# Performance work log

Hardware: AMD Instinct MI355X
Metric: run time of the kernel (lower is better)

The kernel has to match this reference:

```python
import jax, jax.numpy as jnp
import numpy as np

B, T, F, U = 64, 512, 32, 64
EPS = 1e-3  # keras LayerNormalization default epsilon


def _ln(x, g, b):
    m = jnp.mean(x, axis=-1, keepdims=True)
    v = jnp.var(x, axis=-1, keepdims=True)
    return (x - m) / jnp.sqrt(v + EPS) * g + b


def setup_inputs() -> dict:
    key = jax.random.key(0)
    ks = jax.random.split(key, 24)
    s = 0.05
    inp = {
        "x": jax.random.normal(ks[0], (B, T, F), dtype=jnp.float32),
        # per-feature GRNs, stacked over F (each sub-net has independent params)
        "W1": jax.random.normal(ks[1], (F, U), jnp.float32) * s,   # dense_1 (1->U)
        "b1": jnp.zeros((F, U), jnp.float32),
        "W2": jax.random.normal(ks[2], (F, U, U), jnp.float32) * s,  # dense_2 (U->U)
        "b2": jnp.zeros((F, U), jnp.float32),
        "Wg1": jax.random.normal(ks[3], (F, U, U), jnp.float32) * s,  # GLU linear
        "bg1": jnp.zeros((F, U), jnp.float32),
        "Wg2": jax.random.normal(ks[4], (F, U, U), jnp.float32) * s,  # GLU gate
        "bg2": jnp.zeros((F, U), jnp.float32),
        "Wp": jax.random.normal(ks[5], (F, U), jnp.float32) * s,   # project (1->U)
        "bp": jnp.zeros((F, U), jnp.float32),
        "gamma": jnp.ones((F, U), jnp.float32),
        "beta": jnp.zeros((F, U), jnp.float32),
        # weights GRN (F -> F, no projection since in_dim == units == F)
        "w1w": jax.random.normal(ks[6], (F, F), jnp.float32) * s,
        "b1w": jnp.zeros((F,), jnp.float32),
        "w2w": jax.random.normal(ks[7], (F, F), jnp.float32) * s,
        "b2w": jnp.zeros((F,), jnp.float32),
        "wg1w": jax.random.normal(ks[8], (F, F), jnp.float32) * s,
        "bg1w": jnp.zeros((F,), jnp.float32),
        "wg2w": jax.random.normal(ks[9], (F, F), jnp.float32) * s,
        "bg2w": jnp.zeros((F,), jnp.float32),
        "gammaw": jnp.ones((F,), jnp.float32),
        "betaw": jnp.zeros((F,), jnp.float32),
    }
    return inp


def reference(x, W1, b1, W2, b2, Wg1, bg1, Wg2, bg2, Wp, bp, gamma, beta,
              w1w, b1w, w2w, b2w, wg1w, bg1w, wg2w, bg2w, gammaw, betaw):
    # ---- variable weights GRN on flattened features (input dim F == units F, no projection) ----
    h = jax.nn.elu(jnp.einsum('btf,fg->btg', x, w1w) + b1w)
    h = jnp.einsum('btf,fg->btg', h, w2w) + b2w
    g = (jnp.einsum('btf,fg->btg', h, wg1w) + bg1w) * jax.nn.sigmoid(
        jnp.einsum('btf,fg->btg', h, wg2w) + bg2w)
    w = _ln(g + x, gammaw, betaw)
    w = jax.nn.softmax(w, axis=-1)  # [B,T,F]

    # ---- per-feature GRNs, batched over F (scalar input per feature) ----
    xe = x[..., None]                                   # [B,T,F,1]
    res = xe * Wp + bp                                  # project residual [B,T,F,U]
    h = jax.nn.elu(xe * W1 + b1)                        # dense_1 [B,T,F,U]
    h = jnp.einsum('btfu,fuv->btfv', h, W2) + b2        # dense_2
    g = (jnp.einsum('btfu,fuv->btfv', h, Wg1) + bg1) * jax.nn.sigmoid(
        jnp.einsum('btfu,fuv->btfv', h, Wg2) + bg2)     # GLU
    y = _ln(g + res, gamma, beta)                       # [B,T,F,U]

    out = jnp.einsum('btfu,btf->btu', y, w)             # softmax-weighted sum over features
    return out, w
```

## Files before the change

kernel.cpp:

```cpp
#include <hip/hip_runtime.h>
#include <hip/hip_bf16.h>


typedef float f4      __attribute__((ext_vector_type(4)));
typedef float f2      __attribute__((ext_vector_type(2)));
typedef float f32x4   __attribute__((ext_vector_type(4)));
typedef short bf16x8  __attribute__((ext_vector_type(8)));
typedef unsigned short u16x4 __attribute__((ext_vector_type(4)));
typedef unsigned short u16x8 __attribute__((ext_vector_type(8)));

#define N_ROWS 32768
#define F_DIM  32
#define U_DIM  64
#define RPB    16
#define NTHR   256
#define NBLK   (N_ROWS / RPB)

#define PHA_FRAG 49152
#define VECT_BYTE_OFF 794624

#define X_OFF   0
#define WT_OFF  2304
#define VA_OFF  3584
#define SMEM_BYTES 16384

__device__ __forceinline__ unsigned short bfu(float x) {
  union { __hip_bfloat16 h; unsigned short u; } c;
  c.h = __float2bfloat16(x);
  return c.u;
}
__device__ __forceinline__ float bf2f(unsigned short u) {
  union { float f; unsigned v; } c; c.v = ((unsigned)u) << 16; return c.f;
}

__global__ __launch_bounds__(256) void vsn_prep(
    const float* __restrict__ W2,  const float* __restrict__ Wg1, const float* __restrict__ Wg2,
    const float* __restrict__ W1,  const float* __restrict__ b1,  const float* __restrict__ b2,
    const float* __restrict__ bg1, const float* __restrict__ bg2,
    const float* __restrict__ Wp,  const float* __restrict__ bp,
    const float* __restrict__ gamma_, const float* __restrict__ beta_,
    const float* __restrict__ w1w, const float* __restrict__ w2w,
    const float* __restrict__ wg1w, const float* __restrict__ wg2w,
    unsigned short* __restrict__ wtg, float* __restrict__ vect)
{
  const int t = threadIdx.x, blk = blockIdx.x;
  if (blk < 192) {
    const int m = blk >> 6;
    const int f = (blk >> 1) & 31;
    const int half = blk & 1;
    const float* src = (m == 0) ? W2 : (m == 1) ? Wg1 : Wg2;
    src += f * 4096;
    const int c  = half * 256 + t;
    const int nt = c >> 7;
    const int rr = c & 127;
    const int kt = rr >> 6;
    const int ln = rr & 63;
    const int g  = ln >> 4, lrr = ln & 15;
    const int uo = lrr + 16 * nt;
    u16x8 tmp;
    if (m == 0) {
      #pragma unroll
      for (int j = 0; j < 8; ++j)
        tmp[j] = bfu(src[(8 * g + 32 * kt + j) * 64 + uo]);
    } else {
      #pragma unroll
      for (int j = 0; j < 8; ++j)
        tmp[j] = bfu(src[(4 * g + (j & 3) + 16 * (j >> 2) + 32 * kt) * 64 + uo]);
    }
    *(u16x8*)(wtg + ((size_t)(m * 32 + f) * 512 + c) * 8) = tmp;
  } else if (blk < 194) {
    const int h = blk - 192;
    for (int i = h * 1024 + t; i < (h + 1) * 1024; i += 256) {
      const int f = i >> 6, u = i & 63;
      float* vf = vect + f * 576;
      vf[u]              = W1[i];
      vf[64 + u]         = b1[i];
      vf[128 + u]        = b2[i];
      vf[192 + u * 4 + 0] = bg1[i];
      vf[192 + u * 4 + 1] = bg2[i];
      vf[192 + u * 4 + 2] = Wp[i];
      vf[192 + u * 4 + 3] = bp[i];
      vf[448 + u * 2 + 0] = gamma_[i];
      vf[448 + u * 2 + 1] = beta_[i];
    }
  } else {
    #pragma unroll
    for (int cc = 0; cc < 2; ++cc) {
      const int q = t + cc * 256;
      const int mat = q >> 7;
      const int nt  = (q >> 6) & 1;
      const int ln  = q & 63;
      const int lr  = ln & 15, lg = ln >> 4;
      const float* src = (mat == 0) ? w1w : (mat == 1) ? w2w : (mat == 2) ? wg1w : wg2w;
      u16x8 tmp;
      if (mat == 0) {
        #pragma unroll
        for (int j = 0; j < 8; ++j)
          tmp[j] = bfu(src[(8 * lg + j) * 32 + lr + 16 * nt]);
      } else {
        #pragma unroll
        for (int j = 0; j < 8; ++j)
          tmp[j] = bfu(src[(4 * lg + (j & 3) + 16 * (j >> 2)) * 32 + lr + 16 * nt]);
      }
      *(u16x8*)(wtg + ((size_t)PHA_FRAG + q) * 8) = tmp;
    }
  }
}

__global__ __launch_bounds__(NTHR, 4) void vsn_main(
    const float* __restrict__ x,
    const unsigned short* __restrict__ wtg,
    const float* __restrict__ vect,
    const float* __restrict__ b1w, const float* __restrict__ b2w,
    const float* __restrict__ bg1w, const float* __restrict__ bg2w,
    const float* __restrict__ gammaw, const float* __restrict__ betaw,
    float* __restrict__ out, float* __restrict__ wout)
{
  __shared__ __align__(16) char smem[SMEM_BYTES];
  const int t  = threadIdx.x;
  const int r0 = blockIdx.x * RPB;

  float* xt  = (float*)(smem + X_OFF);
  unsigned short* wtlb = (unsigned short*)(smem + WT_OFF);
  float* vAl = (float*)(smem + VA_OFF);

  const int wid  = t >> 6;
  const int lane = t & 63;
  const int lr   = lane & 15;
  const int lg   = lane >> 4;
  const int fbase = wid * 8;

  if (t < 128) {
    f4 v = ((const f4*)(x + (size_t)r0 * F_DIM))[t];
    *((f4*)(xt + (t >> 3) * 36 + ((t & 7) << 2))) = v;
  }
  if (t < 48) {
    int m = t >> 3, off = (t & 7) << 2;
    const float* src = (m==0)?b1w:(m==1)?b2w:(m==2)?bg1w:(m==3)?bg2w:(m==4)?gammaw:betaw;
    *(f4*)(vAl + m * 32 + off) = *((const f4*)(src + off));
  }
  __syncthreads();

  {
    const bf16x8* pf = ((const bf16x8*)wtg) + PHA_FRAG;

    f4 xa0 = *(const f4*)(xt + lr * 36 + 8 * lg);
    f4 xa1 = *(const f4*)(xt + lr * 36 + 8 * lg + 4);
    bf16x8 xb;
    #pragma unroll
    for (int j = 0; j < 4; ++j) { xb[j] = (short)bfu(xa0[j]); xb[4 + j] = (short)bfu(xa1[j]); }

    f32x4 c1a[2];
    #pragma unroll
    for (int nt = 0; nt < 2; ++nt)
      c1a[nt] = __builtin_amdgcn_mfma_f32_16x16x32_bf16(
          pf[(0 * 2 + nt) * 64 + lane], xb, (f32x4){0.f,0.f,0.f,0.f}, 0, 0, 0);
    float hv[8];
    #pragma unroll
    for (int nt = 0; nt < 2; ++nt)
      #pragma unroll
      for (int rg = 0; rg < 4; ++rg) {
        const int g = 4 * lg + rg + 16 * nt;
        float h = c1a[nt][rg] + vAl[g];
        hv[nt * 4 + rg] = h > 0.f ? h : (__expf(h) - 1.f);
      }
    bf16x8 hf;
    #pragma unroll
    for (int j = 0; j < 8; ++j) hf[j] = (short)bfu(hv[j]);

    f32x4 c2a[2];
    #pragma unroll
    for (int nt = 0; nt < 2; ++nt)
      c2a[nt] = __builtin_amdgcn_mfma_f32_16x16x32_bf16(
          pf[(1 * 2 + nt) * 64 + lane], hf, (f32x4){0.f,0.f,0.f,0.f}, 0, 0, 0);
    bf16x8 h2f;
    #pragma unroll
    for (int nt = 0; nt < 2; ++nt)
      #pragma unroll
      for (int rg = 0; rg < 4; ++rg) {
        const int g = 4 * lg + rg + 16 * nt;
        h2f[nt * 4 + rg] = (short)bfu(c2a[nt][rg] + vAl[32 + g]);
      }

    f32x4 cga[2], cgb[2];
    #pragma unroll
    for (int nt = 0; nt < 2; ++nt) {
      cga[nt] = __builtin_amdgcn_mfma_f32_16x16x32_bf16(
          pf[(2 * 2 + nt) * 64 + lane], h2f, (f32x4){0.f,0.f,0.f,0.f}, 0, 0, 0);
      cgb[nt] = __builtin_amdgcn_mfma_f32_16x16x32_bf16(
          pf[(3 * 2 + nt) * 64 + lane], h2f, (f32x4){0.f,0.f,0.f,0.f}, 0, 0, 0);
    }
    float zv[8];
    float s1 = 0.f, s2 = 0.f;
    #pragma unroll
    for (int nt = 0; nt < 2; ++nt)
      #pragma unroll
      for (int rg = 0; rg < 4; ++rg) {
        const int g = 4 * lg + rg + 16 * nt;
        float a = cga[nt][rg] + vAl[64 + g];
        float b = cgb[nt][rg] + vAl[96 + g];
        float sg = __builtin_amdgcn_rcpf(1.f + __expf(-b));
        float z = a * sg + xt[lr * 36 + g];
        zv[nt * 4 + rg] = z;
        s1 += z; s2 += z * z;
      }
    s1 += __shfl_xor(s1, 16, 64); s1 += __shfl_xor(s1, 32, 64);
    s2 += __shfl_xor(s2, 16, 64); s2 += __shfl_xor(s2, 32, 64);
    const float mA = s1 * 0.03125f;
    const float vA = s2 * 0.03125f - mA * mA;
    const float rsA = __builtin_amdgcn_rsqf(vA + 1e-3f);
    float yv[8], mx = -1e30f;
    #pragma unroll
    for (int nt = 0; nt < 2; ++nt)
      #pragma unroll
      for (int rg = 0; rg < 4; ++rg) {
        const int g = 4 * lg + rg + 16 * nt;
        float y = (zv[nt * 4 + rg] - mA) * rsA * vAl[128 + g] + vAl[160 + g];
        yv[nt * 4 + rg] = y;
        mx = fmaxf(mx, y);
      }
    mx = fmaxf(mx, __shfl_xor(mx, 16, 64));
    mx = fmaxf(mx, __shfl_xor(mx, 32, 64));
    float ev[8], es = 0.f;
    #pragma unroll
    for (int j = 0; j < 8; ++j) { ev[j] = __expf(yv[j] - mx); es += ev[j]; }
    es += __shfl_xor(es, 16, 64); es += __shfl_xor(es, 32, 64);
    const float inv = __builtin_amdgcn_rcpf(es);
    #pragma unroll
    for (int nt = 0; nt < 2; ++nt)
      #pragma unroll
      for (int rg = 0; rg < 4; ++rg) {
        const int g = 4 * lg + rg + 16 * nt;
        wtlb[lr * 40 + g] = bfu(ev[nt * 4 + rg] * inv);
      }
    if (t < 128) {
      const int row = t >> 3, c4 = (t & 7) << 2;
      u16x4 wq = *(const u16x4*)(wtlb + row * 40 + c4);
      f4 wo = { bf2f(wq[0]), bf2f(wq[1]), bf2f(wq[2]), bf2f(wq[3]) };
      *(f4*)(wout + (size_t)(r0 + row) * 32 + c4) = wo;
    }
  }

  const bf16x8* wf = (const bf16x8*)wtg;

  f32x4 acc[4];
  #pragma unroll
  for (int nt = 0; nt < 4; ++nt) acc[nt] = (f32x4){0.f, 0.f, 0.f, 0.f};

  for (int i = 0; i < 8; ++i) {
    const int f = fbase + i;
    const float* vb = vect + f * 576;

    const int base0 = (0 * 32 + f) * 512 + lane;
    bf16x8 w2f[8];
    #pragma unroll
    for (int nt = 0; nt < 4; ++nt)
      #pragma unroll
      for (int kt = 0; kt < 2; ++kt)
        w2f[nt * 2 + kt] = wf[base0 + nt * 128 + kt * 64];

    const float s_ = xt[lr * 36 + f];
    bf16x8 afr[2];
    #pragma unroll
    for (int kt = 0; kt < 2; ++kt) {
      const int u0 = 8 * lg + 32 * kt;
      f4 wa  = *(const f4*)(vb + u0);
      f4 wb_ = *(const f4*)(vb + u0 + 4);
      f4 ba  = *(const f4*)(vb + 64 + u0);
      f4 bb_ = *(const f4*)(vb + 64 + u0 + 4);
      bf16x8 af;
      #pragma unroll
      for (int j = 0; j < 4; ++j) {
        float h = s_ * wa[j] + ba[j];
        h = h > 0.f ? h : (__expf(h) - 1.f);
        af[j] = (short)bfu(h);
      }
      #pragma unroll
      for (int j = 0; j < 4; ++j) {
        float h = s_ * wb_[j] + bb_[j];
        h = h > 0.f ? h : (__expf(h) - 1.f);
        af[4 + j] = (short)bfu(h);
      }
      afr[kt] = af;
    }

    f32x4 c1[4];
    #pragma unroll
    for (int nt = 0; nt < 4; ++nt) {
      c1[nt] = (f32x4){0.f, 0.f, 0.f, 0.f};
      #pragma unroll
      for (int kt = 0; kt < 2; ++kt)
        c1[nt] = __builtin_amdgcn_mfma_f32_16x16x32_bf16(w2f[nt * 2 + kt], afr[kt], c1[nt], 0, 0, 0);
    }

    f4 b2q[4];
    #pragma unroll
    for (int kt = 0; kt < 2; ++kt)
      #pragma unroll
      for (int n2 = 0; n2 < 2; ++n2)
        b2q[n2 + 2 * kt] = *(const f4*)(vb + 128 + 4 * lg + 16 * n2 + 32 * kt);
    bf16x8 a2[2];
    #pragma unroll
    for (int kt = 0; kt < 2; ++kt) {
      bf16x8 af;
      #pragma unroll
      for (int j = 0; j < 8; ++j) {
        const int q = (j >> 2) + 2 * kt;
        af[j] = (short)bfu(c1[q][j & 3] + b2q[q][j & 3]);
      }
      a2[kt] = af;
    }

    const int base1 = (1 * 32 + f) * 512 + lane;
    bf16x8 bfa[8];
    #pragma unroll
    for (int nt = 0; nt < 4; ++nt)
      #pragma unroll
      for (int kt = 0; kt < 2; ++kt)
        bfa[nt * 2 + kt] = wf[base1 + nt * 128 + kt * 64];
    f32x4 ca[4], cb[4];
    #pragma unroll
    for (int nt = 0; nt < 4; ++nt) {
      ca[nt] = (f32x4){0.f,0.f,0.f,0.f};
      #pragma unroll
      for (int kt = 0; kt < 2; ++kt)
        ca[nt] = __builtin_amdgcn_mfma_f32_16x16x32_bf16(a2[kt], bfa[nt * 2 + kt], ca[nt], 0, 0, 0);
    }

    const int base2 = (2 * 32 + f) * 512 + lane;
    bf16x8 bfb[8];
    #pragma unroll
    for (int nt = 0; nt < 4; ++nt)
      #pragma unroll
      for (int kt = 0; kt < 2; ++kt)
        bfb[nt * 2 + kt] = wf[base2 + nt * 128 + kt * 64];
    #pragma unroll
    for (int nt = 0; nt < 4; ++nt) {
      cb[nt] = (f32x4){0.f,0.f,0.f,0.f};
      #pragma unroll
      for (int kt = 0; kt < 2; ++kt)
        cb[nt] = __builtin_amdgcn_mfma_f32_16x16x32_bf16(a2[kt], bfb[nt * 2 + kt], cb[nt], 0, 0, 0);
    }

    float xr[4], wr[4];
    #pragma unroll
    for (int rg = 0; rg < 4; ++rg) {
      const int rl = 4 * lg + rg;
      xr[rg] = xt[rl * 36 + f];
      wr[rg] = bf2f(wtlb[rl * 40 + f]);
    }
    float zf[4][4];
    float s1[4] = {0.f,0.f,0.f,0.f}, s2[4] = {0.f,0.f,0.f,0.f};
    #pragma unroll
    for (int nt = 0; nt < 4; ++nt) {
      const int u = lr + 16 * nt;
      f4 Q = *(const f4*)(vb + 192 + u * 4);
      #pragma unroll
      for (int rg = 0; rg < 4; ++rg) {
        float a = ca[nt][rg] + Q[0];
        float b = cb[nt][rg] + Q[1];
        float sg = __builtin_amdgcn_rcpf(1.f + __expf(-b));
        float z = a * sg + (xr[rg] * Q[2] + Q[3]);
        zf[nt][rg] = z;
        s1[rg] += z;
        s2[rg] += z * z;
      }
    }
    #pragma unroll
    for (int rg = 0; rg < 4; ++rg) {
      #pragma unroll
      for (int m = 1; m < 16; m <<= 1) {
        s1[rg] += __shfl_xor(s1[rg], m, 64);
        s2[rg] += __shfl_xor(s2[rg], m, 64);
      }
    }
    float rswr[4], nc2[4];
    #pragma unroll
    for (int rg = 0; rg < 4; ++rg) {
      float mn = s1[rg] * 0.015625f;
      float var = s2[rg] * 0.015625f - mn * mn;
      float rs = __builtin_amdgcn_rsqf(var + 1e-3f);
      rswr[rg] = rs * wr[rg];
      nc2[rg]  = -mn * rswr[rg];
    }
    #pragma unroll
    for (int nt = 0; nt < 4; ++nt) {
      const int u = lr + 16 * nt;
      f2 G = *(const f2*)(vb + 448 + u * 2);
      #pragma unroll
      for (int rg = 0; rg < 4; ++rg) {
        float tm = rswr[rg] * zf[nt][rg] + nc2[rg];
        acc[nt][rg] += G.x * tm + G.y * wr[rg];
      }
    }
  }

  __syncthreads();
  float* cmb = (float*)smem;
  #pragma unroll
  for (int nt = 0; nt < 4; ++nt)
    #pragma unroll
    for (int rg = 0; rg < 4; ++rg)
      cmb[wid * 1024 + (4 * lg + rg) * 64 + lr + 16 * nt] = acc[nt][rg];
  __syncthreads();
  {
    const f4* cmb4 = (const f4*)cmb;
    f4 o = cmb4[t] + cmb4[256 + t] + cmb4[512 + t] + cmb4[768 + t];
    ((f4*)(out + (size_t)r0 * U_DIM))[t] = o;
  }
}

extern "C" void kernel_launch(void* const* d_in, const int* in_sizes, int n_in,
                              void* d_out, int out_size, void* d_ws, size_t ws_size,
                              hipStream_t stream)
{
  (void)in_sizes; (void)n_in; (void)out_size; (void)ws_size;
  const float* x    = (const float*)d_in[0];
  const float* W1   = (const float*)d_in[1];
  const float* b1   = (const float*)d_in[2];
  const float* W2   = (const float*)d_in[3];
  const float* b2   = (const float*)d_in[4];
  const float* Wg1  = (const float*)d_in[5];
  const float* bg1  = (const float*)d_in[6];
  const float* Wg2  = (const float*)d_in[7];
  const float* bg2  = (const float*)d_in[8];
  const float* Wp   = (const float*)d_in[9];
  const float* bp   = (const float*)d_in[10];
  const float* gm   = (const float*)d_in[11];
  const float* bt   = (const float*)d_in[12];
  const float* w1w  = (const float*)d_in[13];
  const float* b1w  = (const float*)d_in[14];
  const float* w2w  = (const float*)d_in[15];
  const float* b2w  = (const float*)d_in[16];
  const float* wg1w = (const float*)d_in[17];
  const float* bg1w = (const float*)d_in[18];
  const float* wg2w = (const float*)d_in[19];
  const float* bg2w = (const float*)d_in[20];
  const float* gmw  = (const float*)d_in[21];
  const float* btw  = (const float*)d_in[22];

  unsigned short* wtg = (unsigned short*)d_ws;
  float* vect = (float*)((char*)d_ws + VECT_BYTE_OFF);

  float* out  = (float*)d_out;
  float* wout = out + (size_t)N_ROWS * U_DIM;

  vsn_prep<<<195, 256, 0, stream>>>(W2, Wg1, Wg2, W1, b1, b2, bg1, bg2, Wp, bp, gm, bt,
                                    w1w, w2w, wg1w, wg2w, wtg, vect);
  vsn_main<<<NBLK, NTHR, 0, stream>>>(x, wtg, vect,
                                      b1w, b2w, bg1w, bg2w, gmw, btw, out, wout);
}
```

Baseline: 214.7 us.

## Fold biases into MFMA accumulators, use exp2 sigmoid, stage per-feature vectors in LDS

Biases are now loaded as the initial MFMA accumulator instead of being added afterwards. The gate weights and biases are pre-scaled by -log2(e) in the prep kernel, so the sigmoid can use exp2 directly. The MFMA operand order in the GLU is swapped so each lane holds a single row; this reduces the LayerNorm reduction to two cross-lane shuffles instead of per-row 16-lane butterflies. Per-feature parameter vectors are re-laid out contiguously, prefetched into registers one feature ahead and staged in LDS, which removes scattered global loads from the inner loop. In exchange it costs more LDS and adds register pressure from the prefetch, and the final combine buffer is padded to avoid bank conflicts.

```diff
diff --git a/kernel.cpp b/kernel.cpp
--- a/kernel.cpp
+++ b/kernel.cpp
@@ -3,7 +3,6 @@
 
 
 typedef float f4      __attribute__((ext_vector_type(4)));
-typedef float f2      __attribute__((ext_vector_type(2)));
 typedef float f32x4   __attribute__((ext_vector_type(4)));
 typedef short bf16x8  __attribute__((ext_vector_type(8)));
 typedef unsigned short u16x4 __attribute__((ext_vector_type(4)));
@@ -15,6 +14,7 @@
 #define RPB    16
 #define NTHR   256
 #define NBLK   (N_ROWS / RPB)
+#define LOG2E  1.4426950408889634f
 
 #define PHA_FRAG 49152
 #define VECT_BYTE_OFF 794624
@@ -22,7 +22,8 @@
 #define X_OFF   0
 #define WT_OFF  2304
 #define VA_OFF  3584
-#define SMEM_BYTES 16384
+#define VST_OFF 4352
+#define SMEM_BYTES 17408
 
 __device__ __forceinline__ unsigned short bfu(float x) {
   union { __hip_bfloat16 h; unsigned short u; } c;
@@ -50,6 +51,7 @@
     const int half = blk & 1;
     const float* src = (m == 0) ? W2 : (m == 1) ? Wg1 : Wg2;
     src += f * 4096;
+    const float sc = (m == 2) ? -LOG2E : 1.0f;
     const int c  = half * 256 + t;
     const int nt = c >> 7;
     const int rr = c & 127;
@@ -65,7 +67,7 @@
     } else {
       #pragma unroll
       for (int j = 0; j < 8; ++j)
-        tmp[j] = bfu(src[(4 * g + (j & 3) + 16 * (j >> 2) + 32 * kt) * 64 + uo]);
+        tmp[j] = bfu(src[(4 * g + (j & 3) + 16 * (j >> 2) + 32 * kt) * 64 + uo] * sc);
     }
     *(u16x8*)(wtg + ((size_t)(m * 32 + f) * 512 + c) * 8) = tmp;
   } else if (blk < 194) {
@@ -73,15 +75,15 @@
     for (int i = h * 1024 + t; i < (h + 1) * 1024; i += 256) {
       const int f = i >> 6, u = i & 63;
       float* vf = vect + f * 576;
-      vf[u]              = W1[i];
-      vf[64 + u]         = b1[i];
-      vf[128 + u]        = b2[i];
-      vf[192 + u * 4 + 0] = bg1[i];
-      vf[192 + u * 4 + 1] = bg2[i];
-      vf[192 + u * 4 + 2] = Wp[i];
-      vf[192 + u * 4 + 3] = bp[i];
-      vf[448 + u * 2 + 0] = gamma_[i];
-      vf[448 + u * 2 + 1] = beta_[i];
+      vf[u]       = W1[i];
+      vf[64 + u]  = b1[i];
+      vf[128 + u] = b2[i];
+      vf[192 + u] = bg1[i];
+      vf[256 + u] = bg2[i] * (-LOG2E);
+      vf[320 + u] = Wp[i];
+      vf[384 + u] = bp[i];
+      vf[448 + u] = gamma_[i];
+      vf[512 + u] = beta_[i];
     }
   } else {
     #pragma unroll
@@ -92,6 +94,7 @@
       const int ln  = q & 63;
       const int lr  = ln & 15, lg = ln >> 4;
       const float* src = (mat == 0) ? w1w : (mat == 1) ? w2w : (mat == 2) ? wg1w : wg2w;
+      const float sc = (mat == 3) ? -LOG2E : 1.0f;
       u16x8 tmp;
       if (mat == 0) {
         #pragma unroll
@@ -100,7 +103,7 @@
       } else {
         #pragma unroll
         for (int j = 0; j < 8; ++j)
-          tmp[j] = bfu(src[(4 * lg + (j & 3) + 16 * (j >> 2)) * 32 + lr + 16 * nt]);
+          tmp[j] = bfu(src[(4 * lg + (j & 3) + 16 * (j >> 2)) * 32 + lr + 16 * nt] * sc);
       }
       *(u16x8*)(wtg + ((size_t)PHA_FRAG + q) * 8) = tmp;
     }
@@ -123,6 +126,7 @@
   float* xt  = (float*)(smem + X_OFF);
   unsigned short* wtlb = (unsigned short*)(smem + WT_OFF);
   float* vAl = (float*)(smem + VA_OFF);
+  float* vstf = (float*)(smem + VST_OFF);
 
   const int wid  = t >> 6;
   const int lane = t & 63;
@@ -137,9 +141,23 @@
   if (t < 48) {
     int m = t >> 3, off = (t & 7) << 2;
     const float* src = (m==0)?b1w:(m==1)?b2w:(m==2)?bg1w:(m==3)?bg2w:(m==4)?gammaw:betaw;
-    *(f4*)(vAl + m * 32 + off) = *((const f4*)(src + off));
-  }
+    f4 v = *((const f4*)(src + off));
+    if (m == 3) { v[0]*=-LOG2E; v[1]*=-LOG2E; v[2]*=-LOG2E; v[3]*=-LOG2E; }
+    *(f4*)(vAl + m * 32 + off) = v;
+  }
+
+  const f4* vect4 = (const f4*)vect;
+  f4 rv0 = vect4[fbase * 144 + lane];
+  f4 rv1 = vect4[fbase * 144 + 64 + lane];
+  f4 rv2 = {};
+  if (lane < 16) rv2 = vect4[fbase * 144 + 128 + lane];
+
   __syncthreads();
+
+  f4* vst4 = ((f4*)vstf) + wid * 144;
+  float* vsc = vstf + wid * 576;
+  vst4[lane] = rv0; vst4[64 + lane] = rv1;
+  if (lane < 16) vst4[128 + lane] = rv2;
 
   {
     const bf16x8* pf = ((const bf16x8*)wtg) + PHA_FRAG;
@@ -154,53 +172,49 @@
     #pragma unroll
     for (int nt = 0; nt < 2; ++nt)
       c1a[nt] = __builtin_amdgcn_mfma_f32_16x16x32_bf16(
-          pf[(0 * 2 + nt) * 64 + lane], xb, (f32x4){0.f,0.f,0.f,0.f}, 0, 0, 0);
-    float hv[8];
+          pf[(0 * 2 + nt) * 64 + lane], xb,
+          *(const f32x4*)(vAl + 4 * lg + 16 * nt), 0, 0, 0);
+    bf16x8 hf;
+    #pragma unroll
+    for (int nt = 0; nt < 2; ++nt)
+      #pragma unroll
+      for (int rg = 0; rg < 4; ++rg) {
+        float h = c1a[nt][rg];
+        hf[nt * 4 + rg] = (short)bfu(h > 0.f ? h : (__expf(h) - 1.f));
+      }
+
+    f32x4 c2a[2];
+    #pragma unroll
+    for (int nt = 0; nt < 2; ++nt)
+      c2a[nt] = __builtin_amdgcn_mfma_f32_16x16x32_bf16(
+          pf[(1 * 2 + nt) * 64 + lane], hf,
+          *(const f32x4*)(vAl + 32 + 4 * lg + 16 * nt), 0, 0, 0);
+    bf16x8 h2f;
+    #pragma unroll
+    for (int nt = 0; nt < 2; ++nt)
+      #pragma unroll
+      for (int rg = 0; rg < 4; ++rg)
+        h2f[nt * 4 + rg] = (short)bfu(c2a[nt][rg]);
+
+    f32x4 cga[2], cgb[2];
+    #pragma unroll
+    for (int nt = 0; nt < 2; ++nt) {
+      cga[nt] = __builtin_amdgcn_mfma_f32_16x16x32_bf16(
+          pf[(2 * 2 + nt) * 64 + lane], h2f,
+          *(const f32x4*)(vAl + 64 + 4 * lg + 16 * nt), 0, 0, 0);
+      cgb[nt] = __builtin_amdgcn_mfma_f32_16x16x32_bf16(
+          pf[(3 * 2 + nt) * 64 + lane], h2f,
+          *(const f32x4*)(vAl + 96 + 4 * lg + 16 * nt), 0, 0, 0);
+    }
+    float zv[8];
+    float s1 = 0.f, s2 = 0.f;
     #pragma unroll
     for (int nt = 0; nt < 2; ++nt)
       #pragma unroll
       for (int rg = 0; rg < 4; ++rg) {
         const int g = 4 * lg + rg + 16 * nt;
-        float h = c1a[nt][rg] + vAl[g];
-        hv[nt * 4 + rg] = h > 0.f ? h : (__expf(h) - 1.f);
-      }
-    bf16x8 hf;
-    #pragma unroll
-    for (int j = 0; j < 8; ++j) hf[j] = (short)bfu(hv[j]);
-
-    f32x4 c2a[2];
-    #pragma unroll
-    for (int nt = 0; nt < 2; ++nt)
-      c2a[nt] = __builtin_amdgcn_mfma_f32_16x16x32_bf16(
-          pf[(1 * 2 + nt) * 64 + lane], hf, (f32x4){0.f,0.f,0.f,0.f}, 0, 0, 0);
-    bf16x8 h2f;
-    #pragma unroll
-    for (int nt = 0; nt < 2; ++nt)
-      #pragma unroll
-      for (int rg = 0; rg < 4; ++rg) {
-        const int g = 4 * lg + rg + 16 * nt;
-        h2f[nt * 4 + rg] = (short)bfu(c2a[nt][rg] + vAl[32 + g]);
-      }
-
-    f32x4 cga[2], cgb[2];
-    #pragma unroll
-    for (int nt = 0; nt < 2; ++nt) {
-      cga[nt] = __builtin_amdgcn_mfma_f32_16x16x32_bf16(
-          pf[(2 * 2 + nt) * 64 + lane], h2f, (f32x4){0.f,0.f,0.f,0.f}, 0, 0, 0);
-      cgb[nt] = __builtin_amdgcn_mfma_f32_16x16x32_bf16(
-          pf[(3 * 2 + nt) * 64 + lane], h2f, (f32x4){0.f,0.f,0.f,0.f}, 0, 0, 0);
-    }
-    float zv[8];
-    float s1 = 0.f, s2 = 0.f;
-    #pragma unroll
-    for (int nt = 0; nt < 2; ++nt)
-      #pragma unroll
-      for (int rg = 0; rg < 4; ++rg) {
-        const int g = 4 * lg + rg + 16 * nt;
-        float a = cga[nt][rg] + vAl[64 + g];
-        float b = cgb[nt][rg] + vAl[96 + g];
-        float sg = __builtin_amdgcn_rcpf(1.f + __expf(-b));
-        float z = a * sg + xt[lr * 36 + g];
+        float sg = __builtin_amdgcn_rcpf(1.f + __builtin_amdgcn_exp2f(cgb[nt][rg]));
+        float z = cga[nt][rg] * sg + xt[lr * 36 + g];
         zv[nt * 4 + rg] = z;
         s1 += z; s2 += z * z;
       }
@@ -249,7 +263,6 @@
 
   for (int i = 0; i < 8; ++i) {
     const int f = fbase + i;
-    const float* vb = vect + f * 576;
 
     const int base0 = (0 * 32 + f) * 512 + lane;
     bf16x8 w2f[8];
@@ -264,10 +277,10 @@
     #pragma unroll
     for (int kt = 0; kt < 2; ++kt) {
       const int u0 = 8 * lg + 32 * kt;
-      f4 wa  = *(const f4*)(vb + u0);
-      f4 wb_ = *(const f4*)(vb + u0 + 4);
-      f4 ba  = *(const f4*)(vb + 64 + u0);
-      f4 bb_ = *(const f4*)(vb + 64 + u0 + 4);
+      f4 wa  = *(const f4*)(vsc + u0);
+      f4 wb_ = *(const f4*)(vsc + u0 + 4);
+      f4 ba  = *(const f4*)(vsc + 64 + u0);
+      f4 bb_ = *(const f4*)(vsc + 64 + u0 + 4);
       bf16x8 af;
       #pragma unroll
       for (int j = 0; j < 4; ++j) {
@@ -287,27 +300,19 @@
     f32x4 c1[4];
     #pragma unroll
     for (int nt = 0; nt < 4; ++nt) {
-      c1[nt] = (f32x4){0.f, 0.f, 0.f, 0.f};
+      c1[nt] = *(const f32x4*)(vsc + 128 + 4 * lg + 16 * nt);
       #pragma unroll
       for (int kt = 0; kt < 2; ++kt)
         c1[nt] = __builtin_amdgcn_mfma_f32_16x16x32_bf16(w2f[nt * 2 + kt], afr[kt], c1[nt], 0, 0, 0);
     }
 
-    f4 b2q[4];
-    #pragma unroll
-    for (int kt = 0; kt < 2; ++kt)
-      #pragma unroll
-      for (int n2 = 0; n2 < 2; ++n2)
-        b2q[n2 + 2 * kt] = *(const f4*)(vb + 128 + 4 * lg + 16 * n2 + 32 * kt);
     bf16x8 a2[2];
     #pragma unroll
     for (int kt = 0; kt < 2; ++kt) {
       bf16x8 af;
       #pragma unroll
-      for (int j = 0; j < 8; ++j) {
-        const int q = (j >> 2) + 2 * kt;
-        af[j] = (short)bfu(c1[q][j & 3] + b2q[q][j & 3]);
-      }
+      for (int j = 0; j < 8; ++j)
+        af[j] = (short)bfu(c1[(j >> 2) + 2 * kt][j & 3]);
       a2[kt] = af;
     }
 
@@ -321,10 +326,10 @@
     f32x4 ca[4], cb[4];
     #pragma unroll
     for (int nt = 0; nt < 4; ++nt) {
-      ca[nt] = (f32x4){0.f,0.f,0.f,0.f};
-      #pragma unroll
-      for (int kt = 0; kt < 2; ++kt)
-        ca[nt] = __builtin_amdgcn_mfma_f32_16x16x32_bf16(a2[kt], bfa[nt * 2 + kt], ca[nt], 0, 0, 0);
+      ca[nt] = *(const f32x4*)(vsc + 192 + 16 * nt + 4 * lg);
+      #pragma unroll
+      for (int kt = 0; kt < 2; ++kt)
+        ca[nt] = __builtin_amdgcn_mfma_f32_16x16x32_bf16(bfa[nt * 2 + kt], a2[kt], ca[nt], 0, 0, 0);
     }
 
     const int base2 = (2 * 32 + f) * 512 + lane;
@@ -336,62 +341,53 @@
         bfb[nt * 2 + kt] = wf[base2 + nt * 128 + kt * 64];
     #pragma unroll
     for (int nt = 0; nt < 4; ++nt) {
-      cb[nt] = (f32x4){0.f,0.f,0.f,0.f};
-      #pragma unroll
-      for (int kt = 0; kt < 2; ++kt)
-        cb[nt] = __builtin_amdgcn_mfma_f32_16x16x32_bf16(a2[kt], bfb[nt * 2 + kt], cb[nt], 0, 0, 0);
-    }
-
-    float xr[4], wr[4];
-    #pragma unroll
-    for (int rg = 0; rg < 4; ++rg) {
-      const int rl = 4 * lg + rg;
-      xr[rg] = xt[rl * 36 + f];
-      wr[rg] = bf2f(wtlb[rl * 40 + f]);
-    }
+      cb[nt] = *(const f32x4*)(vsc + 256 + 16 * nt + 4 * lg);
+      #pragma unroll
+      for (int kt = 0; kt < 2; ++kt)
+        cb[nt] = __builtin_amdgcn_mfma_f32_16x16x32_bf16(bfb[nt * 2 + kt], a2[kt], cb[nt], 0, 0, 0);
+    }
+
+    if (i < 7) {
+      rv0 = vect4[(f + 1) * 144 + lane];
+      rv1 = vect4[(f + 1) * 144 + 64 + lane];
+      if (lane < 16) rv2 = vect4[(f + 1) * 144 + 128 + lane];
+    }
+
+    const float wr_ = bf2f(wtlb[lr * 40 + f]);
     float zf[4][4];
-    float s1[4] = {0.f,0.f,0.f,0.f}, s2[4] = {0.f,0.f,0.f,0.f};
+    float s1 = 0.f, s2 = 0.f;
     #pragma unroll
     for (int nt = 0; nt < 4; ++nt) {
-      const int u = lr + 16 * nt;
-      f4 Q = *(const f4*)(vb + 192 + u * 4);
+      f4 wp4 = *(const f4*)(vsc + 320 + 16 * nt + 4 * lg);
+      f4 bp4 = *(const f4*)(vsc + 384 + 16 * nt + 4 * lg);
       #pragma unroll
       for (int rg = 0; rg < 4; ++rg) {
-        float a = ca[nt][rg] + Q[0];
-        float b = cb[nt][rg] + Q[1];
-        float sg = __builtin_amdgcn_rcpf(1.f + __expf(-b));
-        float z = a * sg + (xr[rg] * Q[2] + Q[3]);
+        float sg = __builtin_amdgcn_rcpf(1.f + __builtin_amdgcn_exp2f(cb[nt][rg]));
+        float z = ca[nt][rg] * sg + (s_ * wp4[rg] + bp4[rg]);
         zf[nt][rg] = z;
-        s1[rg] += z;
-        s2[rg] += z * z;
-      }
-    }
-    #pragma unroll
-    for (int rg = 0; rg < 4; ++rg) {
-      #pragma unroll
-      for (int m = 1; m < 16; m <<= 1) {
-        s1[rg] += __shfl_xor(s1[rg], m, 64);
-        s2[rg] += __shfl_xor(s2[rg], m, 64);
-      }
-    }
-    float rswr[4], nc2[4];
-    #pragma unroll
-    for (int rg = 0; rg < 4; ++rg) {
-      float mn = s1[rg] * 0.015625f;
-      float var = s2[rg] * 0.015625f - mn * mn;
-      float rs = __builtin_amdgcn_rsqf(var + 1e-3f);
-      rswr[rg] = rs * wr[rg];
-      nc2[rg]  = -mn * rswr[rg];
-    }
+        s1 += z;
+        s2 += z * z;
+      }
+    }
+    s1 += __shfl_xor(s1, 16, 64); s1 += __shfl_xor(s1, 32, 64);
+    s2 += __shfl_xor(s2, 16, 64); s2 += __shfl_xor(s2, 32, 64);
+    const float mn = s1 * 0.015625f;
+    const float var = s2 * 0.015625f - mn * mn;
+    const float rs = __builtin_amdgcn_rsqf(var + 1e-3f);
+    const float rswr = rs * wr_;
+    const float nc2 = -mn * rswr;
     #pragma unroll
     for (int nt = 0; nt < 4; ++nt) {
-      const int u = lr + 16 * nt;
-      f2 G = *(const f2*)(vb + 448 + u * 2);
-      #pragma unroll
-      for (int rg = 0; rg < 4; ++rg) {
-        float tm = rswr[rg] * zf[nt][rg] + nc2[rg];
-        acc[nt][rg] += G.x * tm + G.y * wr[rg];
-      }
+      f4 g4 = *(const f4*)(vsc + 448 + 16 * nt + 4 * lg);
+      f4 b4 = *(const f4*)(vsc + 512 + 16 * nt + 4 * lg);
+      #pragma unroll
+      for (int rg = 0; rg < 4; ++rg)
+        acc[nt][rg] += g4[rg] * (rswr * zf[nt][rg] + nc2) + b4[rg] * wr_;
+    }
+
+    if (i < 7) {
+      vst4[lane] = rv0; vst4[64 + lane] = rv1;
+      if (lane < 16) vst4[128 + lane] = rv2;
     }
   }
 
@@ -399,14 +395,14 @@
   float* cmb = (float*)smem;
   #pragma unroll
   for (int nt = 0; nt < 4; ++nt)
-    #pragma unroll
-    for (int rg = 0; rg < 4; ++rg)
-      cmb[wid * 1024 + (4 * lg + rg) * 64 + lr + 16 * nt] = acc[nt][rg];
+    *(f4*)(cmb + wid * 1088 + lr * 68 + 16 * nt + 4 * lg) = acc[nt];
   __syncthreads();
   {
-    const f4* cmb4 = (const f4*)cmb;
-    f4 o = cmb4[t] + cmb4[256 + t] + cmb4[512 + t] + cmb4[768 + t];
-    ((f4*)(out + (size_t)r0 * U_DIM))[t] = o;
+    const int row = t >> 4, u4 = (t & 15) << 2;
+    const float* cp = cmb + row * 68 + u4;
+    f4 o = *(const f4*)(cp) + *(const f4*)(cp + 1088) +
+           *(const f4*)(cp + 2176) + *(const f4*)(cp + 3264);
+    *(f4*)(out + (size_t)(r0 + row) * U_DIM + u4) = o;
   }
 }
 
```

Result: faster. 178.5 us (-16.8%).
